# Optimization experiments

Hardware: AMD Instinct MI355X
Metric: run time of the kernel (lower is better)

## Reference

```python
import jax, jax.numpy as jnp
import numpy as np

# parameter limits (low, high) as in Filter_param.limits
LIMITS = {
    'f_start': (200.0, 4000.0),
    'f_inf': (20.0, 500.0),
    'f_decay': (0.0, 2.0),
    'f_T': (0.0, 2.0),
    'w_offset': (0.0, 1.0),
    'w_T': (0.01, 0.5),
}

B, T = 2048, 8192

def setup_inputs() -> dict:
    key = jax.random.key(0)
    ks = jax.random.split(key, 7)
    return {
        'X': jax.random.normal(ks[0], (B, T), dtype=jnp.float32),
        'F': 44100,  # sampling frequency (int constant)
        'f_start_normal': jax.random.normal(ks[1], (), dtype=jnp.float32),
        'f_inf_normal': jax.random.normal(ks[2], (), dtype=jnp.float32),
        'f_decay_normal': jax.random.normal(ks[3], (), dtype=jnp.float32),
        'f_T_normal': jax.random.normal(ks[4], (), dtype=jnp.float32),
        'w_offset_normal': jax.random.normal(ks[5], (), dtype=jnp.float32),
        'w_T_normal': jax.random.normal(ks[6], (), dtype=jnp.float32),
    }

def _squash(v, name):
    low, high = LIMITS[name]
    return low + (high - low) * jax.nn.sigmoid(v)

def reference(X, F, f_start_normal, f_inf_normal, f_decay_normal,
              f_T_normal, w_offset_normal, w_T_normal):
    Bsz, Tlen = X.shape
    c = (2.0 ** (1.0 / 3.0) - 1.0) ** 0.5 * F / np.pi  # scalar cutoff constant
    t = jnp.arange(Tlen, dtype=X.dtype) / Tlen  # normalized time [T]

    f_start = _squash(f_start_normal, 'f_start')
    f_inf = _squash(f_inf_normal, 'f_inf')
    f_decay = _squash(f_decay_normal, 'f_decay')
    f_T = _squash(f_T_normal, 'f_T')
    w_offset = _squash(w_offset_normal, 'w_offset')
    w_T = _squash(w_T_normal, 'w_T')

    # time-varying cutoff frequency and output window
    f = f_inf + (f_start - f_inf) * (0.7 * 0.1 ** f_decay) ** (t / (10.0 * 0.1 ** f_T))  # [T]
    w = jax.nn.sigmoid((t - w_offset) / w_T)  # [T]
    a = (f - c) / (f + c)  # [T]
    b = (a + 1.0) / 2.0    # [T]

    # cascaded time-varying one-pole recurrence (two stages), scanned over time.
    # t=0: y1 = y2 = X[:,0];   t>0:
    #   y1[t] = b[t]*(x[t] + x[t-1]) - a[t]*y1[t-1]
    #   y2[t] = b[t]*(y1[t] + y1[t-1]) - a[t]*y2[t-1]
    x0 = X[:, 0]
    init = (x0, x0, x0, w[0] * x0)  # (y0_prev, y1_prev, y2_prev, acc)

    def step(carry, inp):
        y0p, y1p, y2p, acc = carry
        x_t, a_t, b_t, w_t = inp
        y1 = b_t * (x_t + y0p) - a_t * y1p
        y2 = b_t * (y1 + y1p) - a_t * y2p
        return (x_t, y1, y2, acc + w_t * y2), None

    xs = (X[:, 1:].T, a[1:], b[1:], w[1:])  # time-major [T-1, ...]
    (_, _, _, acc), _ = jax.lax.scan(step, init, xs)

    return acc / jnp.sum(w)  # prediction [B]
```

## Files before the change

### kernel.cpp

```cpp
#include <hip/hip_runtime.h>
#include <math.h>

#define BB 2048
#define TT 8192
#define NSEG 128
#define SL 64

__device__ inline float sigmoid_dev(float v) { return 1.0f / (1.0f + __expf(-v)); }
__device__ inline float squash_dev(float v, float lo, float hi) {
    return lo + (hi - lo) * sigmoid_dev(v);
}

struct SquashedParams {
    float c, f_start, f_inf, log2K_invTd, w_offset, inv_w_T;
};

__device__ inline SquashedParams load_params(const int* Fp,
                                             const float* p_fstart, const float* p_finf,
                                             const float* p_fdecay, const float* p_fT,
                                             const float* p_woff, const float* p_wT) {
    SquashedParams P;
    float Fv      = (float)(*Fp);
    P.c           = sqrtf(exp2f(1.0f / 3.0f) - 1.0f) * Fv / 3.14159265358979323846f;
    P.f_start     = squash_dev(*p_fstart, 200.0f, 4000.0f);
    P.f_inf       = squash_dev(*p_finf,   20.0f,  500.0f);
    float f_decay = squash_dev(*p_fdecay, 0.0f,   2.0f);
    float f_T     = squash_dev(*p_fT,     0.0f,   2.0f);
    P.w_offset    = squash_dev(*p_woff,   0.0f,   1.0f);
    float w_T     = squash_dev(*p_wT,     0.01f,  0.5f);
    P.inv_w_T     = 1.0f / w_T;
    const float LOG2_10 = 3.32192809488736235f;
    float log2K  = log2f(0.7f) - LOG2_10 * f_decay;
    float invTd  = 0.1f * exp2f(LOG2_10 * f_T);
    P.log2K_invTd = log2K * invTd;
    return P;
}

__global__ __launch_bounds__(256, 4)
void fused_kernel(const float* __restrict__ X,
                  const int* Fp,
                  const float* p_fstart, const float* p_finf,
                  const float* p_fdecay, const float* p_fT,
                  const float* p_woff, const float* p_wT,
                  float* __restrict__ out) {
    const int tid  = threadIdx.x;
    const int lane = tid & 63;
    const int wid  = tid >> 6;
    const int rloc = wid >> 1;
    const int half = wid & 1;
    const int row  = (blockIdx.x << 1) + rloc;
    const int seg  = (half << 6) + lane;

    SquashedParams P = load_params(Fp, p_fstart, p_finf, p_fdecay, p_fT, p_woff, p_wT);

    const float* base = X + (size_t)row * TT + seg * SL;
    float e[SL];
    #pragma unroll
    for (int i = 0; i < SL / 4; i++) {
        float4 v = reinterpret_cast<const float4*>(base)[i];
        e[4 * i + 0] = v.x; e[4 * i + 1] = v.y;
        e[4 * i + 2] = v.z; e[4 * i + 3] = v.w;
    }
    float xn = __shfl_down(e[0], 1);
    if (lane == 63 && seg < NSEG - 1) xn = base[SL];

    const float dti     = 1.0f / (float)TT;
    const float ti_base = (float)(seg * SL + 1) * dti;
    const float df      = P.f_start - P.f_inf;
    float ef = exp2f(P.log2K_invTd * ti_base);
    const float cf = exp2f(P.log2K_invTd * dti);
    float ew = __expf(-(ti_base - P.w_offset) * P.inv_w_T);
    const float cw = __expf(-dti * P.inv_w_T);

    float y1 = 0.0f, y2 = 0.0f, q3 = 0.0f;
    float al = 1.0f, be = 0.0f, ga = 0.0f, de = 0.0f, ws = 0.0f;
    #pragma unroll
    for (int k = 0; k < SL; k++) {
        float f  = fmaf(df, ef, P.f_inf);
        ef *= cf;
        float r  = __builtin_amdgcn_rcpf(f + P.c);
        float b  = f * r;
        float m  = (P.c - f) * r;
        float p  = b * (1.0f + m);
        float w  = __builtin_amdgcn_rcpf(1.0f + ew);
        ew *= cw;
        if (seg == NSEG - 1 && k == SL - 1) { m = 0.0f; b = 0.0f; p = 0.0f; w = 0.0f; }

        float x  = (k < SL - 1) ? e[k + 1] : xn;
        float u  = b * (x + e[k]);
        float y2n = fmaf(m, y2, fmaf(p, y1, b * u));
        y1 = fmaf(m, y1, u);
        y2 = y2n;
        q3 = fmaf(w, y2n, q3);

        float nal = m * al;
        float nbe = fmaf(p, al, m * be);
        de = fmaf(w * m, al, de);
        ga = fmaf(w, nbe, ga);
        al = nal; be = nbe;
        ws += w;
    }
    float q1 = y1, q2 = y2;

    #pragma unroll
    for (int o = 1; o < 64; o <<= 1) {
        float al2 = __shfl_down(al, o);
        float be2 = __shfl_down(be, o);
        float ga2 = __shfl_down(ga, o);
        float de2 = __shfl_down(de, o);
        float q12 = __shfl_down(q1, o);
        float q22 = __shfl_down(q2, o);
        float q32 = __shfl_down(q3, o);
        float ws2 = __shfl_down(ws, o);
        float nal = al2 * al;
        float nbe = fmaf(be2, al, al2 * be);
        float nga = fmaf(ga2, al, fmaf(de2, be, ga));
        float nde = fmaf(de2, al, de);
        float nq1 = fmaf(al2, q1, q12);
        float nq2 = fmaf(be2, q1, fmaf(al2, q2, q22));
        float nq3 = fmaf(ga2, q1, fmaf(de2, q2, q3 + q32));
        al = nal; be = nbe; ga = nga; de = nde;
        q1 = nq1; q2 = nq2; q3 = nq3; ws += ws2;
    }

    __shared__ float sred[4][8];
    __shared__ float sx0[2];
    if (lane == 0) {
        sred[wid][0] = al; sred[wid][1] = be; sred[wid][2] = ga; sred[wid][3] = de;
        sred[wid][4] = q1; sred[wid][5] = q2; sred[wid][6] = q3; sred[wid][7] = ws;
        if (half == 0) sx0[rloc] = e[0];
    }
    __syncthreads();

    if (tid < 2) {
        int r = tid;
        const float* E = sred[2 * r + 0];
        const float* L = sred[2 * r + 1];
        float alE = E[0], beE = E[1], gaE = E[2], deE = E[3];
        float q1E = E[4], q2E = E[5], q3E = E[6];
        float gaL = L[2], deL = L[3], q3L = L[6];
        float ga_f = fmaf(gaL, alE, fmaf(deL, beE, gaE));
        float de_f = fmaf(deL, alE, deE);
        float q3_f = fmaf(gaL, q1E, fmaf(deL, q2E, q3E + q3L));
        float x0 = sx0[r];
        float w0 = sigmoid_dev((0.0f - P.w_offset) * P.inv_w_T);
        float sumw = E[7] + L[7] + w0;
        float accf = fmaf(ga_f + de_f + w0, x0, q3_f);
        out[(blockIdx.x << 1) + r] = accf / sumw;
    }
}

extern "C" void kernel_launch(void* const* d_in, const int* in_sizes, int n_in,
                              void* d_out, int out_size, void* d_ws, size_t ws_size,
                              hipStream_t stream) {
    const float* X        = (const float*)d_in[0];
    const int*   Fp       = (const int*)d_in[1];
    const float* p_fstart = (const float*)d_in[2];
    const float* p_finf   = (const float*)d_in[3];
    const float* p_fdecay = (const float*)d_in[4];
    const float* p_fT     = (const float*)d_in[5];
    const float* p_woff   = (const float*)d_in[6];
    const float* p_wT     = (const float*)d_in[7];
    float* out = (float*)d_out;

    fused_kernel<<<BB / 2, 256, 0, stream>>>(X, Fp, p_fstart, p_finf, p_fdecay,
                                             p_fT, p_woff, p_wT, out);
}
```

Baseline: 110.6 us.

## Stream input in double-buffered chunks and simplify recurrence coefficient math

```diff
diff --git a/kernel.cpp b/kernel.cpp
--- a/kernel.cpp
+++ b/kernel.cpp
@@ -5,6 +5,8 @@
 #define TT 8192
 #define NSEG 128
 #define SL 64
+#define CH 16
+#define NCH (SL/CH)
 
 __device__ inline float sigmoid_dev(float v) { return 1.0f / (1.0f + __expf(-v)); }
 __device__ inline float squash_dev(float v, float lo, float hi) {
@@ -54,14 +56,16 @@
     SquashedParams P = load_params(Fp, p_fstart, p_finf, p_fdecay, p_fT, p_woff, p_wT);
 
     const float* base = X + (size_t)row * TT + seg * SL;
-    float e[SL];
+
+    float eb[2][CH];
     #pragma unroll
-    for (int i = 0; i < SL / 4; i++) {
+    for (int i = 0; i < CH / 4; i++) {
         float4 v = reinterpret_cast<const float4*>(base)[i];
-        e[4 * i + 0] = v.x; e[4 * i + 1] = v.y;
-        e[4 * i + 2] = v.z; e[4 * i + 3] = v.w;
+        eb[0][4 * i + 0] = v.x; eb[0][4 * i + 1] = v.y;
+        eb[0][4 * i + 2] = v.z; eb[0][4 * i + 3] = v.w;
     }
-    float xn = __shfl_down(e[0], 1);
+    float x_first = eb[0][0];
+    float xn = __shfl_down(x_first, 1);
     if (lane == 63 && seg < NSEG - 1) xn = base[SL];
 
     const float dti     = 1.0f / (float)TT;
@@ -75,30 +79,45 @@
     float y1 = 0.0f, y2 = 0.0f, q3 = 0.0f;
     float al = 1.0f, be = 0.0f, ga = 0.0f, de = 0.0f, ws = 0.0f;
     #pragma unroll
-    for (int k = 0; k < SL; k++) {
-        float f  = fmaf(df, ef, P.f_inf);
-        ef *= cf;
-        float r  = __builtin_amdgcn_rcpf(f + P.c);
-        float b  = f * r;
-        float m  = (P.c - f) * r;
-        float p  = b * (1.0f + m);
-        float w  = __builtin_amdgcn_rcpf(1.0f + ew);
-        ew *= cw;
-        if (seg == NSEG - 1 && k == SL - 1) { m = 0.0f; b = 0.0f; p = 0.0f; w = 0.0f; }
+    for (int c = 0; c < NCH; c++) {
+        const int cur = c & 1, nxt = cur ^ 1;
+        if (c < NCH - 1) {
+            #pragma unroll
+            for (int i = 0; i < CH / 4; i++) {
+                float4 v = reinterpret_cast<const float4*>(base)[(c + 1) * (CH / 4) + i];
+                eb[nxt][4 * i + 0] = v.x; eb[nxt][4 * i + 1] = v.y;
+                eb[nxt][4 * i + 2] = v.z; eb[nxt][4 * i + 3] = v.w;
+            }
+        }
+        #pragma unroll
+        for (int k = 0; k < CH; k++) {
+            const int kg = c * CH + k;
+            float f  = fmaf(df, ef, P.f_inf);
+            ef *= cf;
+            float r  = __builtin_amdgcn_rcpf(f + P.c);
+            float b  = f * r;
+            float m  = fmaf(-2.0f, b, 1.0f);
+            float p  = fmaf(b, m, b);
+            float w  = __builtin_amdgcn_rcpf(1.0f + ew);
+            ew *= cw;
+            if (seg == NSEG - 1 && kg == SL - 1) { m = 0.0f; b = 0.0f; p = 0.0f; w = 0.0f; }
 
-        float x  = (k < SL - 1) ? e[k + 1] : xn;
-        float u  = b * (x + e[k]);
-        float y2n = fmaf(m, y2, fmaf(p, y1, b * u));
-        y1 = fmaf(m, y1, u);
-        y2 = y2n;
-        q3 = fmaf(w, y2n, q3);
+            float x   = (k < CH - 1) ? eb[cur][k + 1]
+                      : ((c < NCH - 1) ? eb[nxt][0] : xn);
+            float u   = b * (x + eb[cur][k]);
+            float y1n = fmaf(m, y1, u);
+            float vs  = y1n + y1;
+            float y2n = fmaf(m, y2, b * vs);
+            y1 = y1n; y2 = y2n;
+            q3 = fmaf(w, y2n, q3);
 
-        float nal = m * al;
-        float nbe = fmaf(p, al, m * be);
-        de = fmaf(w * m, al, de);
-        ga = fmaf(w, nbe, ga);
-        al = nal; be = nbe;
-        ws += w;
+            float nal = m * al;
+            float nbe = fmaf(p, al, m * be);
+            de = fmaf(w, nal, de);
+            ga = fmaf(w, nbe, ga);
+            al = nal; be = nbe;
+            ws += w;
+        }
     }
     float q1 = y1, q2 = y2;
 
@@ -128,7 +147,7 @@
     if (lane == 0) {
         sred[wid][0] = al; sred[wid][1] = be; sred[wid][2] = ga; sred[wid][3] = de;
         sred[wid][4] = q1; sred[wid][5] = q2; sred[wid][6] = q3; sred[wid][7] = ws;
-        if (half == 0) sx0[rloc] = e[0];
+        if (half == 0) sx0[rloc] = x_first;
     }
     __syncthreads();
 
```

Result: slower. 144.7 us (+30.9%).
